# Kernel tuning notes

Hardware: AMD Instinct MI355X
Metric: run time of the kernel (lower is better)

## Reference

```python
import jax, jax.numpy as jnp
import numpy as np

EPS = 1e-5
B, N, K = 2, 40960, 16
D_OUT = 64
H = D_OUT // 2  # 32

PNAMES = ['mlp1_w','mlp1_b','mlp1_g','mlp1_beta','mlp1_m','mlp1_v',
          'ap1_fc_w','ap1_fc_b','ap1_mlp_w','ap1_mlp_b','ap1_g','ap1_beta','ap1_m','ap1_v',
          'mlp2_w','mlp2_b','mlp2_g','mlp2_beta','mlp2_m','mlp2_v',
          'ap2_fc_w','ap2_fc_b','ap2_mlp_w','ap2_mlp_b','ap2_g','ap2_beta','ap2_m','ap2_v']


def _conv1x1(x, w, b):
    # x: (B,C,N,K), w: (O,C) -> (B,O,N,K)
    return jnp.einsum('oc,bcnk->bonk', w, x) + b[None, :, None, None]


def _bn(x, g, beta, m, v):
    # eval-mode BatchNorm2d over channel axis 1
    scale = g / jnp.sqrt(v + EPS)
    return (x - m[None, :, None, None]) * scale[None, :, None, None] + beta[None, :, None, None]


def _gather_neighbour(pc, idx):
    # pc: (B,N,d), idx: (B,N,K) -> (B,N,K,d)
    b, n, d = pc.shape
    k = idx.shape[-1]
    flat = idx.reshape(b, n * k)
    feats = jnp.take_along_axis(pc, flat[:, :, None], axis=1)  # (B,N*K,d)
    return feats.reshape(b, n, k, d)


def _rel_pos_enc(xyz, idx):
    nbr = _gather_neighbour(xyz, idx)                       # (B,N,K,3)
    tile = jnp.broadcast_to(xyz[:, :, None, :], nbr.shape)  # (B,N,K,3)
    rel = tile - nbr
    dist = jnp.sqrt(jnp.sum(rel * rel, axis=-1, keepdims=True))
    return jnp.concatenate([dist, rel, tile, nbr], axis=-1)  # (B,N,K,10)


def _att_pool(f, fc_w, fc_b, mw, mb, g, beta, m, v):
    # f: (B,C,N,K)
    att = jax.nn.relu(_conv1x1(f, fc_w, fc_b))
    scores = jax.nn.softmax(att, axis=3)
    agg = jnp.sum(f * scores, axis=3, keepdims=True)        # (B,C,N,1)
    return jax.nn.relu(_bn(_conv1x1(agg, mw, mb), g, beta, m, v))


def _forward(xyz, feature, neigh_idx, p):
    # relative pos encoding -> (B,10,N,K)
    f_xyz = _rel_pos_enc(xyz, neigh_idx).transpose(0, 3, 1, 2)
    f_xyz = jax.nn.relu(_bn(_conv1x1(f_xyz, p['mlp1_w'], p['mlp1_b']),
                            p['mlp1_g'], p['mlp1_beta'], p['mlp1_m'], p['mlp1_v']))  # (B,H,N,K)
    f_nb = _gather_neighbour(feature[..., 0].transpose(0, 2, 1), neigh_idx).transpose(0, 3, 1, 2)  # (B,H,N,K)
    f_cat = jnp.concatenate([f_nb, f_xyz], axis=1)          # (B,D_OUT,N,K)
    f_agg = _att_pool(f_cat, p['ap1_fc_w'], p['ap1_fc_b'], p['ap1_mlp_w'], p['ap1_mlp_b'],
                      p['ap1_g'], p['ap1_beta'], p['ap1_m'], p['ap1_v'])  # (B,H,N,1)
    f_xyz = jax.nn.relu(_bn(_conv1x1(f_xyz, p['mlp2_w'], p['mlp2_b']),
                            p['mlp2_g'], p['mlp2_beta'], p['mlp2_m'], p['mlp2_v']))  # (B,H,N,K)
    f_nb = _gather_neighbour(f_agg[..., 0].transpose(0, 2, 1), neigh_idx).transpose(0, 3, 1, 2)  # (B,H,N,K)
    f_cat = jnp.concatenate([f_nb, f_xyz], axis=1)          # (B,D_OUT,N,K)
    return _att_pool(f_cat, p['ap2_fc_w'], p['ap2_fc_b'], p['ap2_mlp_w'], p['ap2_mlp_b'],
                     p['ap2_g'], p['ap2_beta'], p['ap2_m'], p['ap2_v'])  # (B,D_OUT,N,1)


def setup_inputs() -> dict:
    key = jax.random.key(0)
    ks = iter(jax.random.split(key, 64))

    def w(o, c):
        return jax.random.normal(next(ks), (o, c), jnp.float32) * float(np.sqrt(2.0 / c))

    def bias(c):
        return jax.random.normal(next(ks), (c,), jnp.float32) * 0.01

    def bnp(c):
        g = jax.random.uniform(next(ks), (c,), jnp.float32, 0.5, 1.5)
        beta = jax.random.normal(next(ks), (c,), jnp.float32) * 0.1
        m = jax.random.normal(next(ks), (c,), jnp.float32) * 0.1
        v = jax.random.uniform(next(ks), (c,), jnp.float32, 0.5, 1.5)
        return g, beta, m, v

    inp = {}
    inp['xyz'] = jax.random.normal(next(ks), (B, N, 3), jnp.float32)
    inp['feature'] = jax.random.normal(next(ks), (B, H, N, 1), jnp.float32)
    inp['mlp1_w'], inp['mlp1_b'] = w(H, 10), bias(H)
    inp['mlp1_g'], inp['mlp1_beta'], inp['mlp1_m'], inp['mlp1_v'] = bnp(H)
    inp['ap1_fc_w'], inp['ap1_fc_b'] = w(D_OUT, D_OUT), bias(D_OUT)
    inp['ap1_mlp_w'], inp['ap1_mlp_b'] = w(H, D_OUT), bias(H)
    inp['ap1_g'], inp['ap1_beta'], inp['ap1_m'], inp['ap1_v'] = bnp(H)
    inp['mlp2_w'], inp['mlp2_b'] = w(H, H), bias(H)
    inp['mlp2_g'], inp['mlp2_beta'], inp['mlp2_m'], inp['mlp2_v'] = bnp(H)
    inp['ap2_fc_w'], inp['ap2_fc_b'] = w(D_OUT, D_OUT), bias(D_OUT)
    inp['ap2_mlp_w'], inp['ap2_mlp_b'] = w(D_OUT, D_OUT), bias(D_OUT)
    inp['ap2_g'], inp['ap2_beta'], inp['ap2_m'], inp['ap2_v'] = bnp(D_OUT)
    inp['neigh_idx'] = jax.random.randint(next(ks), (B, N, K), 0, N, jnp.int64 if jax.config.jax_enable_x64 else jnp.int32)
    return inp


def reference(xyz, feature, mlp1_w, mlp1_b, mlp1_g, mlp1_beta, mlp1_m, mlp1_v,
              ap1_fc_w, ap1_fc_b, ap1_mlp_w, ap1_mlp_b, ap1_g, ap1_beta, ap1_m, ap1_v,
              mlp2_w, mlp2_b, mlp2_g, mlp2_beta, mlp2_m, mlp2_v,
              ap2_fc_w, ap2_fc_b, ap2_mlp_w, ap2_mlp_b, ap2_g, ap2_beta, ap2_m, ap2_v,
              neigh_idx):
    p = dict(zip(PNAMES, (mlp1_w, mlp1_b, mlp1_g, mlp1_beta, mlp1_m, mlp1_v,
                          ap1_fc_w, ap1_fc_b, ap1_mlp_w, ap1_mlp_b, ap1_g, ap1_beta, ap1_m, ap1_v,
                          mlp2_w, mlp2_b, mlp2_g, mlp2_beta, mlp2_m, mlp2_v,
                          ap2_fc_w, ap2_fc_b, ap2_mlp_w, ap2_mlp_b, ap2_g, ap2_beta, ap2_m, ap2_v)))
    return _forward(xyz, feature, neigh_idx, p)
```

## Files before the change

kernel.cpp:

```cpp
#include <hip/hip_runtime.h>
#include <math.h>

#define BB 2
#define NN 40960
#define KK 16

typedef float v2f __attribute__((ext_vector_type(2)));
__device__ __forceinline__ v2f fma2(v2f a, v2f b, v2f c){
  return __builtin_elementwise_fma(a, b, c);
}
__device__ __forceinline__ v2f mk2(float a, float b){ v2f r; r.x=a; r.y=b; return r; }

template<int CTRL>
__device__ __forceinline__ float dppf(float x){
  return __int_as_float(__builtin_amdgcn_update_dpp(0, __float_as_int(x), CTRL, 0xF, 0xF, true));
}
__device__ __forceinline__ float red16_sum(float v){
  v += dppf<0xB1>(v);
  v += dppf<0x4E>(v);
  v += dppf<0x141>(v);
  v += dppf<0x140>(v);
  return v;
}

__device__ alignas(16) float g_pw1[32*10];
__device__ alignas(16) float g_pb1[32];
__device__ alignas(16) float g_pw2[32*32];
__device__ alignas(16) float g_pb2[32];
__device__ alignas(16) float g_pcw[32*64];
__device__ alignas(16) float g_pcb[32];
__device__ alignas(16) float g_pdw[64*64];
__device__ alignas(16) float g_pdb[64];

__global__ __launch_bounds__(256) void k_pre(
  const float* __restrict__ feat, float* __restrict__ feat_t,
  const float* __restrict__ w1, const float* __restrict__ b1,
  const float* __restrict__ g1, const float* __restrict__ be1, const float* __restrict__ m1, const float* __restrict__ v1,
  const float* __restrict__ w2, const float* __restrict__ b2,
  const float* __restrict__ g2, const float* __restrict__ be2, const float* __restrict__ m2, const float* __restrict__ v2,
  const float* __restrict__ cw, const float* __restrict__ cb,
  const float* __restrict__ cg, const float* __restrict__ cbe, const float* __restrict__ cm, const float* __restrict__ cv,
  const float* __restrict__ dw, const float* __restrict__ db,
  const float* __restrict__ dg, const float* __restrict__ dbe, const float* __restrict__ dm, const float* __restrict__ dv)
{
  int tid = threadIdx.x;
  int bid = blockIdx.x;
  if (bid < BB*NN/256){
    int b = bid / (NN/256);
    int n = (bid % (NN/256))*256 + tid;
    float v[32];
    #pragma unroll
    for (int h=0; h<32; ++h) v[h] = feat[((size_t)(b*32+h))*NN + n];
    float* o = feat_t + ((size_t)b*NN + n)*32;
    #pragma unroll
    for (int h=0; h<32; h+=4){ *(float4*)(o+h) = make_float4(v[h],v[h+1],v[h+2],v[h+3]); }
    return;
  }
  for (int i=tid; i<320; i+=256){ int h=i/10;
    g_pw1[i] = w1[i] * (g1[h]*rsqrtf(v1[h]+1e-5f)); }
  if (tid<32){ float s=g1[tid]*rsqrtf(v1[tid]+1e-5f);
    g_pb1[tid] = (b1[tid]-m1[tid])*s+be1[tid]; }
  for (int i=tid; i<1024; i+=256){ int h=i>>5;
    g_pw2[i] = w2[i] * (g2[h]*rsqrtf(v2[h]+1e-5f)); }
  if (tid<32){ float s=g2[tid]*rsqrtf(v2[tid]+1e-5f);
    g_pb2[tid] = (b2[tid]-m2[tid])*s+be2[tid]; }
  for (int i=tid; i<2048; i+=256){ int h=i>>6;
    g_pcw[i] = cw[i] * (cg[h]*rsqrtf(cv[h]+1e-5f)); }
  if (tid<32){ float s=cg[tid]*rsqrtf(cv[tid]+1e-5f);
    g_pcb[tid] = (cb[tid]-cm[tid])*s+cbe[tid]; }
  for (int i=tid; i<4096; i+=256){ int h=i>>6;
    g_pdw[i] = dw[i] * (dg[h]*rsqrtf(dv[h]+1e-5f)); }
  if (tid<64){ float s=dg[tid]*rsqrtf(dv[tid]+1e-5f);
    g_pdb[tid] = (db[tid]-dm[tid])*s+dbe[tid]; }
}

__global__ __launch_bounds__(256,2) void k_stage1(
  const float* __restrict__ xyz, const float* __restrict__ feat_t, const int* __restrict__ nidx,
  const float* __restrict__ fcw, const float* __restrict__ fcb,
  float* __restrict__ fagg)
{
  int tid = threadIdx.x;
  int lane = tid & 63, wvv = tid >> 6;
  int k = lane & 15, ns = lane >> 4;
  int b = blockIdx.x / (NN/16);
  int n = (blockIdx.x % (NN/16))*16 + wvv*4 + ns;
  size_t bn = (size_t)b*NN + n;
  int idxv = nidx[bn*KK + k];

  alignas(16) float fc_[64];
  const float* fb = feat_t + ((size_t)b*NN + idxv)*32;
  #pragma unroll
  for (int h=0; h<32; h+=4){ float4 x=*(const float4*)(fb+h);
    fc_[h]=x.x; fc_[h+1]=x.y; fc_[h+2]=x.z; fc_[h+3]=x.w; }

  const float* tp = xyz + bn*3;
  const float* qp = xyz + ((size_t)b*NN + idxv)*3;
  float t0=tp[0],t1=tp[1],t2=tp[2];
  float q0=qp[0],q1=qp[1],q2=qp[2];
  float r0=t0-q0,r1=t1-q1,r2=t2-q2;
  v2f e2[5] = { {sqrtf(r0*r0+r1*r1+r2*r2), r0}, {r1,r2}, {t0,t1}, {t2,q0}, {q1,q2} };

  #pragma unroll
  for (int h=0; h<32; ++h){
    const v2f* wr = (const v2f*)(g_pw1 + h*10);
    v2f acc = mk2(g_pb1[h], 0.f);
    #pragma unroll
    for (int c=0; c<5; ++c) acc = fma2(wr[c], e2[c], acc);
    fc_[32+h] = fmaxf(acc.x+acc.y, 0.f);
  }

  const v2f* fv = (const v2f*)fc_;
  float sp4[4], sf4[4];
  #pragma unroll
  for (int ob=0; ob<64; ob+=4){
    const v2f* w0 = (const v2f*)(fcw + ob*64);
    const v2f* w1p = (const v2f*)(fcw + (ob+1)*64);
    const v2f* w2p = (const v2f*)(fcw + (ob+2)*64);
    const v2f* w3p = (const v2f*)(fcw + (ob+3)*64);
    v2f a0=mk2(fcb[ob],0.f), a1=mk2(fcb[ob+1],0.f), a2=mk2(fcb[ob+2],0.f), a3=mk2(fcb[ob+3],0.f);
    #pragma unroll
    for (int c=0; c<32; ++c){
      v2f f = fv[c];
      a0 = fma2(w0[c], f, a0); a1 = fma2(w1p[c], f, a1);
      a2 = fma2(w2p[c], f, a2); a3 = fma2(w3p[c], f, a3);
    }
    float l0=fmaxf(a0.x+a0.y,0.f), l1=fmaxf(a1.x+a1.y,0.f);
    float l2=fmaxf(a2.x+a2.y,0.f), l3=fmaxf(a3.x+a3.y,0.f);
    float p0=__expf(l0), p1=__expf(l1), p2=__expf(l2), p3=__expf(l3);
    float q0v=fc_[ob]*p0, q1v=fc_[ob+1]*p1, q2v=fc_[ob+2]*p2, q3v=fc_[ob+3]*p3;
    float s0=red16_sum(p0), s1=red16_sum(p1), s2=red16_sum(p2), s3=red16_sum(p3);
    float t0v=red16_sum(q0v), t1v=red16_sum(q1v), t2v=red16_sum(q2v), t3v=red16_sum(q3v);
    if ((ob>>2)==k){
      sp4[0]=s0; sp4[1]=s1; sp4[2]=s2; sp4[3]=s3;
      sf4[0]=t0v; sf4[1]=t1v; sf4[2]=t2v; sf4[3]=t3v;
    }
  }
  v2f a01 = mk2(__fdividef(sf4[0],sp4[0]), __fdividef(sf4[1],sp4[1]));
  v2f a23 = mk2(__fdividef(sf4[2],sp4[2]), __fdividef(sf4[3],sp4[3]));

  float o0=0.f, o1=0.f;
  #pragma unroll
  for (int h=0; h<32; h+=2){
    const v2f* wr0 = (const v2f*)(g_pcw + h*64 + 4*k);
    const v2f* wr1 = (const v2f*)(g_pcw + (h+1)*64 + 4*k);
    v2f p0 = fma2(wr0[0], a01, wr0[1]*a23);
    v2f p1 = fma2(wr1[0], a01, wr1[1]*a23);
    float r0v = red16_sum(p0.x + p0.y);
    float r1v = red16_sum(p1.x + p1.y);
    float v0 = fmaxf(r0v + g_pcb[h], 0.f);
    float v1 = fmaxf(r1v + g_pcb[h+1], 0.f);
    if ((h&15)==k){ if (h<16) o0=v0; else o1=v0; }
    if (((h+1)&15)==k){ if (h+1<16) o0=v1; else o1=v1; }
  }
  float* fo = fagg + bn*32;
  fo[k]=o0; fo[k+16]=o1;
}

__global__ __launch_bounds__(256,2) void k_stage2(
  const float* __restrict__ xyz, const float* __restrict__ fagg, const int* __restrict__ nidx,
  const float* __restrict__ fcw, const float* __restrict__ fcb,
  float* __restrict__ outp)
{
  int tid = threadIdx.x;
  int lane = tid & 63, wvv = tid >> 6;
  int k = lane & 15, ns = lane >> 4;
  int b = blockIdx.x / (NN/16);
  int n = (blockIdx.x % (NN/16))*16 + wvv*4 + ns;
  size_t bn = (size_t)b*NN + n;
  int idxv = nidx[bn*KK + k];

  alignas(16) float fc_[64];
  const float* fb = fagg + ((size_t)b*NN + idxv)*32;
  #pragma unroll
  for (int h=0; h<32; h+=4){ float4 x=*(const float4*)(fb+h);
    fc_[h]=x.x; fc_[h+1]=x.y; fc_[h+2]=x.z; fc_[h+3]=x.w; }

  const float* tp = xyz + bn*3;
  const float* qp = xyz + ((size_t)b*NN + idxv)*3;
  float t0=tp[0],t1=tp[1],t2=tp[2];
  float q0=qp[0],q1=qp[1],q2=qp[2];
  float r0=t0-q0,r1=t1-q1,r2=t2-q2;
  v2f e2[5] = { {sqrtf(r0*r0+r1*r1+r2*r2), r0}, {r1,r2}, {t0,t1}, {t2,q0}, {q1,q2} };

  alignas(8) float fx[32];
  #pragma unroll
  for (int h=0; h<32; ++h){
    const v2f* wr = (const v2f*)(g_pw1 + h*10);
    v2f acc = mk2(g_pb1[h], 0.f);
    #pragma unroll
    for (int c=0; c<5; ++c) acc = fma2(wr[c], e2[c], acc);
    fx[h] = fmaxf(acc.x+acc.y, 0.f);
  }

  const v2f* fxv = (const v2f*)fx;
  #pragma unroll
  for (int h=0; h<32; ++h){
    const v2f* wr = (const v2f*)(g_pw2 + h*32);
    v2f acc = mk2(g_pb2[h], 0.f);
    #pragma unroll
    for (int c=0; c<16; ++c) acc = fma2(wr[c], fxv[c], acc);
    fc_[32+h] = fmaxf(acc.x+acc.y, 0.f);
  }

  const v2f* fv = (const v2f*)fc_;
  float sp4[4], sf4[4];
  #pragma unroll
  for (int ob=0; ob<64; ob+=4){
    const v2f* w0 = (const v2f*)(fcw + ob*64);
    const v2f* w1p = (const v2f*)(fcw + (ob+1)*64);
    const v2f* w2p = (const v2f*)(fcw + (ob+2)*64);
    const v2f* w3p = (const v2f*)(fcw + (ob+3)*64);
    v2f a0=mk2(fcb[ob],0.f), a1=mk2(fcb[ob+1],0.f), a2=mk2(fcb[ob+2],0.f), a3=mk2(fcb[ob+3],0.f);
    #pragma unroll
    for (int c=0; c<32; ++c){
      v2f f = fv[c];
      a0 = fma2(w0[c], f, a0); a1 = fma2(w1p[c], f, a1);
      a2 = fma2(w2p[c], f, a2); a3 = fma2(w3p[c], f, a3);
    }
    float l0=fmaxf(a0.x+a0.y,0.f), l1=fmaxf(a1.x+a1.y,0.f);
    float l2=fmaxf(a2.x+a2.y,0.f), l3=fmaxf(a3.x+a3.y,0.f);
    float p0=__expf(l0), p1=__expf(l1), p2=__expf(l2), p3=__expf(l3);
    float q0v=fc_[ob]*p0, q1v=fc_[ob+1]*p1, q2v=fc_[ob+2]*p2, q3v=fc_[ob+3]*p3;
    float s0=red16_sum(p0), s1=red16_sum(p1), s2=red16_sum(p2), s3=red16_sum(p3);
    float t0v=red16_sum(q0v), t1v=red16_sum(q1v), t2v=red16_sum(q2v), t3v=red16_sum(q3v);
    if ((ob>>2)==k){
      sp4[0]=s0; sp4[1]=s1; sp4[2]=s2; sp4[3]=s3;
      sf4[0]=t0v; sf4[1]=t1v; sf4[2]=t2v; sf4[3]=t3v;
    }
  }
  v2f a01 = mk2(__fdividef(sf4[0],sp4[0]), __fdividef(sf4[1],sp4[1]));
  v2f a23 = mk2(__fdividef(sf4[2],sp4[2]), __fdividef(sf4[3],sp4[3]));

  float o4[4];
  #pragma unroll
  for (int h=0; h<64; h+=2){
    const v2f* wr0 = (const v2f*)(g_pdw + h*64 + 4*k);
    const v2f* wr1 = (const v2f*)(g_pdw + (h+1)*64 + 4*k);
    v2f p0 = fma2(wr0[0], a01, wr0[1]*a23);
    v2f p1 = fma2(wr1[0], a01, wr1[1]*a23);
    float r0v = red16_sum(p0.x + p0.y);
    float r1v = red16_sum(p1.x + p1.y);
    float v0 = fmaxf(r0v + g_pdb[h], 0.f);
    float v1 = fmaxf(r1v + g_pdb[h+1], 0.f);
    if ((h&15)==k) o4[h>>4] = v0;
    if (((h+1)&15)==k) o4[(h+1)>>4] = v1;
  }
  #pragma unroll
  for (int j=0; j<4; ++j)
    outp[((size_t)(b*64 + k + 16*j))*NN + n] = o4[j];
}

extern "C" void kernel_launch(void* const* d_in, const int* in_sizes, int n_in,
                              void* d_out, int out_size, void* d_ws, size_t ws_size,
                              hipStream_t stream){
  const float* xyz     = (const float*)d_in[0];
  const float* feature = (const float*)d_in[1];
  const int*   nidx    = (const int*)d_in[30];
  float* feat_t = (float*)d_ws;
  float* fagg   = feat_t + (size_t)BB*NN*32;

  k_pre<<<BB*NN/256 + 1, 256, 0, stream>>>(feature, feat_t,
    (const float*)d_in[2],(const float*)d_in[3],(const float*)d_in[4],(const float*)d_in[5],
    (const float*)d_in[6],(const float*)d_in[7],
    (const float*)d_in[16],(const float*)d_in[17],(const float*)d_in[18],(const float*)d_in[19],
    (const float*)d_in[20],(const float*)d_in[21],
    (const float*)d_in[10],(const float*)d_in[11],(const float*)d_in[12],(const float*)d_in[13],
    (const float*)d_in[14],(const float*)d_in[15],
    (const float*)d_in[24],(const float*)d_in[25],(const float*)d_in[26],(const float*)d_in[27],
    (const float*)d_in[28],(const float*)d_in[29]);
  k_stage1<<<BB*NN/16, 256, 0, stream>>>(xyz, feat_t, nidx,
    (const float*)d_in[8],(const float*)d_in[9], fagg);
  k_stage2<<<BB*NN/16, 256, 0, stream>>>(xyz, fagg, nidx,
    (const float*)d_in[22],(const float*)d_in[23], (float*)d_out);
}
```

Baseline: 438.3 us.

## Use packed fp16 dot2 for attention FC and mlp2, fold log2e into exp2

```diff
diff --git a/kernel.cpp b/kernel.cpp
--- a/kernel.cpp
+++ b/kernel.cpp
@@ -6,10 +6,35 @@
 #define KK 16
 
 typedef float v2f __attribute__((ext_vector_type(2)));
+typedef _Float16 h16;
+typedef h16 h16x2 __attribute__((ext_vector_type(2)));
+
 __device__ __forceinline__ v2f fma2(v2f a, v2f b, v2f c){
   return __builtin_elementwise_fma(a, b, c);
 }
 __device__ __forceinline__ v2f mk2(float a, float b){ v2f r; r.x=a; r.y=b; return r; }
+
+#if __has_builtin(__builtin_amdgcn_fdot2)
+__device__ __forceinline__ float dot2acc(h16x2 w, h16x2 f, float acc){
+  return __builtin_amdgcn_fdot2(w, f, acc, false);
+}
+#else
+__device__ __forceinline__ float dot2acc(h16x2 w, h16x2 f, float acc){
+  return acc + (float)w.x*(float)f.x + (float)w.y*(float)f.y;
+}
+#endif
+#if __has_builtin(__builtin_amdgcn_exp2f)
+__device__ __forceinline__ float exp2fast(float x){ return __builtin_amdgcn_exp2f(x); }
+#else
+__device__ __forceinline__ float exp2fast(float x){ return __expf(x*0.6931471805599453f); }
+#endif
+#if __has_builtin(__builtin_amdgcn_cvt_pkrtz)
+__device__ __forceinline__ h16x2 pkh(float a, float b){
+  return __builtin_bit_cast(h16x2, __builtin_amdgcn_cvt_pkrtz(a,b));
+}
+#else
+__device__ __forceinline__ h16x2 pkh(float a, float b){ h16x2 r; r.x=(h16)a; r.y=(h16)b; return r; }
+#endif
 
 template<int CTRL>
 __device__ __forceinline__ float dppf(float x){
@@ -25,21 +50,29 @@
 
 __device__ alignas(16) float g_pw1[32*10];
 __device__ alignas(16) float g_pb1[32];
-__device__ alignas(16) float g_pw2[32*32];
+__device__ alignas(16) h16x2 g_w2h[32*16];
 __device__ alignas(16) float g_pb2[32];
+__device__ alignas(16) h16x2 g_fch1[64*32];
+__device__ alignas(16) float g_fcb1s[64];
+__device__ alignas(16) h16x2 g_fch2[64*32];
+__device__ alignas(16) float g_fcb2s[64];
 __device__ alignas(16) float g_pcw[32*64];
 __device__ alignas(16) float g_pcb[32];
 __device__ alignas(16) float g_pdw[64*64];
 __device__ alignas(16) float g_pdb[64];
 
+#define LOG2E 1.44269504088896f
+
 __global__ __launch_bounds__(256) void k_pre(
   const float* __restrict__ feat, float* __restrict__ feat_t,
   const float* __restrict__ w1, const float* __restrict__ b1,
   const float* __restrict__ g1, const float* __restrict__ be1, const float* __restrict__ m1, const float* __restrict__ v1,
+  const float* __restrict__ fc1w, const float* __restrict__ fc1b,
+  const float* __restrict__ cw, const float* __restrict__ cb,
+  const float* __restrict__ cg, const float* __restrict__ cbe, const float* __restrict__ cm, const float* __restrict__ cv,
   const float* __restrict__ w2, const float* __restrict__ b2,
   const float* __restrict__ g2, const float* __restrict__ be2, const float* __restrict__ m2, const float* __restrict__ v2,
-  const float* __restrict__ cw, const float* __restrict__ cb,
-  const float* __restrict__ cg, const float* __restrict__ cbe, const float* __restrict__ cm, const float* __restrict__ cv,
+  const float* __restrict__ fc2w, const float* __restrict__ fc2b,
   const float* __restrict__ dw, const float* __restrict__ db,
   const float* __restrict__ dg, const float* __restrict__ dbe, const float* __restrict__ dm, const float* __restrict__ dv)
 {
@@ -60,10 +93,15 @@
     g_pw1[i] = w1[i] * (g1[h]*rsqrtf(v1[h]+1e-5f)); }
   if (tid<32){ float s=g1[tid]*rsqrtf(v1[tid]+1e-5f);
     g_pb1[tid] = (b1[tid]-m1[tid])*s+be1[tid]; }
-  for (int i=tid; i<1024; i+=256){ int h=i>>5;
-    g_pw2[i] = w2[i] * (g2[h]*rsqrtf(v2[h]+1e-5f)); }
+  for (int i=tid; i<512; i+=256){ int h=i>>4, c=i&15;
+    float s=g2[h]*rsqrtf(v2[h]+1e-5f);
+    g_w2h[i] = pkh(w2[h*32+2*c]*s, w2[h*32+2*c+1]*s); }
   if (tid<32){ float s=g2[tid]*rsqrtf(v2[tid]+1e-5f);
     g_pb2[tid] = (b2[tid]-m2[tid])*s+be2[tid]; }
+  for (int i=tid; i<2048; i+=256){ int o=i>>5, c=i&31;
+    g_fch1[i] = pkh(fc1w[o*64+2*c]*LOG2E, fc1w[o*64+2*c+1]*LOG2E);
+    g_fch2[i] = pkh(fc2w[o*64+2*c]*LOG2E, fc2w[o*64+2*c+1]*LOG2E); }
+  if (tid<64){ g_fcb1s[tid] = fc1b[tid]*LOG2E; g_fcb2s[tid] = fc2b[tid]*LOG2E; }
   for (int i=tid; i<2048; i+=256){ int h=i>>6;
     g_pcw[i] = cw[i] * (cg[h]*rsqrtf(cv[h]+1e-5f)); }
   if (tid<32){ float s=cg[tid]*rsqrtf(cv[tid]+1e-5f);
@@ -76,7 +114,6 @@
 
 __global__ __launch_bounds__(256,2) void k_stage1(
   const float* __restrict__ xyz, const float* __restrict__ feat_t, const int* __restrict__ nidx,
-  const float* __restrict__ fcw, const float* __restrict__ fcb,
   float* __restrict__ fagg)
 {
   int tid = threadIdx.x;
@@ -109,25 +146,29 @@
     fc_[32+h] = fmaxf(acc.x+acc.y, 0.f);
   }
 
-  const v2f* fv = (const v2f*)fc_;
+  h16x2 h2[32];
+  #pragma unroll
+  for (int c=0; c<32; ++c) h2[c] = pkh(fc_[2*c], fc_[2*c+1]);
+
   float sp4[4], sf4[4];
   #pragma unroll
   for (int ob=0; ob<64; ob+=4){
-    const v2f* w0 = (const v2f*)(fcw + ob*64);
-    const v2f* w1p = (const v2f*)(fcw + (ob+1)*64);
-    const v2f* w2p = (const v2f*)(fcw + (ob+2)*64);
-    const v2f* w3p = (const v2f*)(fcw + (ob+3)*64);
-    v2f a0=mk2(fcb[ob],0.f), a1=mk2(fcb[ob+1],0.f), a2=mk2(fcb[ob+2],0.f), a3=mk2(fcb[ob+3],0.f);
+    const h16x2* w0 = &g_fch1[(ob+0)*32];
+    const h16x2* w1p = &g_fch1[(ob+1)*32];
+    const h16x2* w2p = &g_fch1[(ob+2)*32];
+    const h16x2* w3p = &g_fch1[(ob+3)*32];
+    float a0=g_fcb1s[ob+0], a1=g_fcb1s[ob+1], a2=g_fcb1s[ob+2], a3=g_fcb1s[ob+3];
     #pragma unroll
     for (int c=0; c<32; ++c){
-      v2f f = fv[c];
-      a0 = fma2(w0[c], f, a0); a1 = fma2(w1p[c], f, a1);
-      a2 = fma2(w2p[c], f, a2); a3 = fma2(w3p[c], f, a3);
+      h16x2 f = h2[c];
+      a0 = dot2acc(w0[c], f, a0); a1 = dot2acc(w1p[c], f, a1);
+      a2 = dot2acc(w2p[c], f, a2); a3 = dot2acc(w3p[c], f, a3);
     }
-    float l0=fmaxf(a0.x+a0.y,0.f), l1=fmaxf(a1.x+a1.y,0.f);
-    float l2=fmaxf(a2.x+a2.y,0.f), l3=fmaxf(a3.x+a3.y,0.f);
-    float p0=__expf(l0), p1=__expf(l1), p2=__expf(l2), p3=__expf(l3);
-    float q0v=fc_[ob]*p0, q1v=fc_[ob+1]*p1, q2v=fc_[ob+2]*p2, q3v=fc_[ob+3]*p3;
+    float p0=exp2fast(fmaxf(a0,0.f)), p1=exp2fast(fmaxf(a1,0.f));
+    float p2=exp2fast(fmaxf(a2,0.f)), p3=exp2fast(fmaxf(a3,0.f));
+    float f0=(float)h2[(ob>>1)+0].x, f1=(float)h2[(ob>>1)+0].y;
+    float f2=(float)h2[(ob>>1)+1].x, f3=(float)h2[(ob>>1)+1].y;
+    float q0v=f0*p0, q1v=f1*p1, q2v=f2*p2, q3v=f3*p3;
     float s0=red16_sum(p0), s1=red16_sum(p1), s2=red16_sum(p2), s3=red16_sum(p3);
     float t0v=red16_sum(q0v), t1v=red16_sum(q1v), t2v=red16_sum(q2v), t3v=red16_sum(q3v);
     if ((ob>>2)==k){
@@ -158,7 +199,6 @@
 
 __global__ __launch_bounds__(256,2) void k_stage2(
   const float* __restrict__ xyz, const float* __restrict__ fagg, const int* __restrict__ nidx,
-  const float* __restrict__ fcw, const float* __restrict__ fcb,
   float* __restrict__ outp)
 {
   int tid = threadIdx.x;
@@ -191,36 +231,43 @@
     for (int c=0; c<5; ++c) acc = fma2(wr[c], e2[c], acc);
     fx[h] = fmaxf(acc.x+acc.y, 0.f);
   }
-
-  const v2f* fxv = (const v2f*)fx;
-  #pragma unroll
-  for (int h=0; h<32; ++h){
-    const v2f* wr = (const v2f*)(g_pw2 + h*32);
-    v2f acc = mk2(g_pb2[h], 0.f);
-    #pragma unroll
-    for (int c=0; c<16; ++c) acc = fma2(wr[c], fxv[c], acc);
-    fc_[32+h] = fmaxf(acc.x+acc.y, 0.f);
-  }
-
-  const v2f* fv = (const v2f*)fc_;
+  h16x2 hx[16];
+  #pragma unroll
+  for (int c=0; c<16; ++c) hx[c] = pkh(fx[2*c], fx[2*c+1]);
+  #pragma unroll
+  for (int h=0; h<32; h+=2){
+    const h16x2* wr0 = &g_w2h[(h+0)*16];
+    const h16x2* wr1 = &g_w2h[(h+1)*16];
+    float a0 = g_pb2[h+0], a1 = g_pb2[h+1];
+    #pragma unroll
+    for (int c=0; c<16; ++c){ h16x2 f=hx[c]; a0=dot2acc(wr0[c],f,a0); a1=dot2acc(wr1[c],f,a1); }
+    fc_[32+h]   = fmaxf(a0, 0.f);
+    fc_[32+h+1] = fmaxf(a1, 0.f);
+  }
+
+  h16x2 h2[32];
+  #pragma unroll
+  for (int c=0; c<32; ++c) h2[c] = pkh(fc_[2*c], fc_[2*c+1]);
+
   float sp4[4], sf4[4];
   #pragma unroll
   for (int ob=0; ob<64; ob+=4){
-    const v2f* w0 = (const v2f*)(fcw + ob*64);
-    const v2f* w1p = (const v2f*)(fcw + (ob+1)*64);
-    const v2f* w2p = (const v2f*)(fcw + (ob+2)*64);
-    const v2f* w3p = (const v2f*)(fcw + (ob+3)*64);
-    v2f a0=mk2(fcb[ob],0.f), a1=mk2(fcb[ob+1],0.f), a2=mk2(fcb[ob+2],0.f), a3=mk2(fcb[ob+3],0.f);
+    const h16x2* w0 = &g_fch2[(ob+0)*32];
+    const h16x2* w1p = &g_fch2[(ob+1)*32];
+    const h16x2* w2p = &g_fch2[(ob+2)*32];
+    const h16x2* w3p = &g_fch2[(ob+3)*32];
+    float a0=g_fcb2s[ob+0], a1=g_fcb2s[ob+1], a2=g_fcb2s[ob+2], a3=g_fcb2s[ob+3];
     #pragma unroll
     for (int c=0; c<32; ++c){
-      v2f f = fv[c];
-      a0 = fma2(w0[c], f, a0); a1 = fma2(w1p[c], f, a1);
-      a2 = fma2(w2p[c], f, a2); a3 = fma2(w3p[c], f, a3);
+      h16x2 f = h2[c];
+      a0 = dot2acc(w0[c], f, a0); a1 = dot2acc(w1p[c], f, a1);
+      a2 = dot2acc(w2p[c], f, a2); a3 = dot2acc(w3p[c], f, a3);
     }
-    float l0=fmaxf(a0.x+a0.y,0.f), l1=fmaxf(a1.x+a1.y,0.f);
-    float l2=fmaxf(a2.x+a2.y,0.f), l3=fmaxf(a3.x+a3.y,0.f);
-    float p0=__expf(l0), p1=__expf(l1), p2=__expf(l2), p3=__expf(l3);
-    float q0v=fc_[ob]*p0, q1v=fc_[ob+1]*p1, q2v=fc_[ob+2]*p2, q3v=fc_[ob+3]*p3;
+    float p0=exp2fast(fmaxf(a0,0.f)), p1=exp2fast(fmaxf(a1,0.f));
+    float p2=exp2fast(fmaxf(a2,0.f)), p3=exp2fast(fmaxf(a3,0.f));
+    float f0=(float)h2[(ob>>1)+0].x, f1=(float)h2[(ob>>1)+0].y;
+    float f2=(float)h2[(ob>>1)+1].x, f3=(float)h2[(ob>>1)+1].y;
+    float q0v=f0*p0, q1v=f1*p1, q2v=f2*p2, q3v=f3*p3;
     float s0=red16_sum(p0), s1=red16_sum(p1), s2=red16_sum(p2), s3=red16_sum(p3);
     float t0v=red16_sum(q0v), t1v=red16_sum(q1v), t2v=red16_sum(q2v), t3v=red16_sum(q3v);
     if ((ob>>2)==k){
@@ -262,14 +309,14 @@
   k_pre<<<BB*NN/256 + 1, 256, 0, stream>>>(feature, feat_t,
     (const float*)d_in[2],(const float*)d_in[3],(const float*)d_in[4],(const float*)d_in[5],
     (const float*)d_in[6],(const float*)d_in[7],
+    (const float*)d_in[8],(const float*)d_in[9],
+    (const float*)d_in[10],(const float*)d_in[11],(const float*)d_in[12],(const float*)d_in[13],
+    (const float*)d_in[14],(const float*)d_in[15],
     (const float*)d_in[16],(const float*)d_in[17],(const float*)d_in[18],(const float*)d_in[19],
     (const float*)d_in[20],(const float*)d_in[21],
-    (const float*)d_in[10],(const float*)d_in[11],(const float*)d_in[12],(const float*)d_in[13],
-    (const float*)d_in[14],(const float*)d_in[15],
+    (const float*)d_in[22],(const float*)d_in[23],
     (const float*)d_in[24],(const float*)d_in[25],(const float*)d_in[26],(const float*)d_in[27],
     (const float*)d_in[28],(const float*)d_in[29]);
-  k_stage1<<<BB*NN/16, 256, 0, stream>>>(xyz, feat_t, nidx,
-    (const float*)d_in[8],(const float*)d_in[9], fagg);
-  k_stage2<<<BB*NN/16, 256, 0, stream>>>(xyz, fagg, nidx,
-    (const float*)d_in[22],(const float*)d_in[23], (float*)d_out);
-}
+  k_stage1<<<BB*NN/16, 256, 0, stream>>>(xyz, feat_t, nidx, fagg);
+  k_stage2<<<BB*NN/16, 256, 0, stream>>>(xyz, fagg, nidx, (float*)d_out);
+}
```

After: 426.5 us. 2.7% less time.
